# Kernel tuning notes

Hardware: AMD Instinct MI355X
Metric: run time of the kernel (lower is better)

Reference implementation:

```python
import jax, jax.numpy as jnp
import numpy as np

B, S, D, H = 4, 2048, 1024, 16
HD = D // H

def setup_inputs() -> dict:
    key = jax.random.key(0)
    ks = jax.random.split(key, 5)
    scale = 1.0 / np.sqrt(D)
    x = jax.random.normal(ks[0], (B, S, D), dtype=jnp.float32)
    w_qkv = jax.random.normal(ks[1], (D, 3 * D), dtype=jnp.float32) * scale
    b_qkv = jax.random.normal(ks[2], (3 * D,), dtype=jnp.float32) * 0.01
    w_proj = jax.random.normal(ks[3], (D, D), dtype=jnp.float32) * scale
    b_proj = jax.random.normal(ks[4], (D,), dtype=jnp.float32) * 0.01
    return {"x": x, "w_qkv": w_qkv, "b_qkv": b_qkv, "w_proj": w_proj, "b_proj": b_proj}

def reference(x, w_qkv, b_qkv, w_proj, b_proj):
    b, s, d = x.shape
    qkv = x @ w_qkv + b_qkv                      # [B,S,3D]
    qkv = qkv.reshape(b, s, 3, H, HD)
    q, k, v = jnp.moveaxis(qkv, 2, 0)            # each [B,S,H,HD]
    q = q.transpose(0, 2, 1, 3)                  # [B,H,S,HD]
    k = k.transpose(0, 2, 1, 3)
    v = v.transpose(0, 2, 1, 3)
    scale = 1.0 / jnp.sqrt(jnp.asarray(HD, dtype=x.dtype))
    scores = jnp.einsum('bhqd,bhkd->bhqk', q, k) * scale
    attn = jax.nn.softmax(scores, axis=-1)
    out = jnp.einsum('bhqk,bhkd->bhqd', attn, v)  # [B,H,S,HD]
    out = out.transpose(0, 2, 1, 3).reshape(b, s, d)
    return out @ w_proj + b_proj
```

## Files before the change

### kernel.cpp

```cpp
#include <hip/hip_runtime.h>

#define B_  4
#define S_  2048
#define D_  1024
#define H_  16
#define HD_ 64
#define M_  (B_*S_)
#define QSCALE 0.1803368801111204f

typedef unsigned short u16;
typedef __bf16 bf16x8 __attribute__((ext_vector_type(8)));
typedef __bf16 bf16x2 __attribute__((ext_vector_type(2)));
typedef float  f32x4  __attribute__((ext_vector_type(4)));
typedef float  f32x16 __attribute__((ext_vector_type(16)));

__device__ __forceinline__ u16 f2bf(float f) {
  unsigned int u = __float_as_uint(f);
  u += 0x7fffu + ((u >> 16) & 1u);
  return (u16)(u >> 16);
}
__device__ __forceinline__ unsigned int packbf2(float lo, float hi) {
#if __has_builtin(__builtin_amdgcn_cvt_pk_bf16_f32)
  union { bf16x2 v; unsigned int u; } c;
  c.v = __builtin_amdgcn_cvt_pk_bf16_f32(lo, hi);
  return c.u;
#else
  return (unsigned int)f2bf(lo) | ((unsigned int)f2bf(hi) << 16);
#endif
}
__device__ __forceinline__ void gld16(const void* g, void* l) {
  __builtin_amdgcn_global_load_lds(
      (const __attribute__((address_space(1))) unsigned int*)g,
      (__attribute__((address_space(3))) unsigned int*)l, 16, 0, 0);
}
#define WAIT_VM8() asm volatile("s_waitcnt vmcnt(8)" ::: "memory")
#define WAIT_VM0() asm volatile("s_waitcnt vmcnt(0)" ::: "memory")
#define MFMA32(a,b,c) __builtin_amdgcn_mfma_f32_32x32x16_bf16(a,b,c,0,0,0)
#define MFMA16(a,b,c) __builtin_amdgcn_mfma_f32_16x16x32_bf16(a,b,c,0,0,0)

__device__ __forceinline__ size_t off16e(int r, int k) {
  return ((size_t)((r >> 7) * 32 + (k >> 5))) * 4096
       + (size_t)((r >> 4) & 7) * 512
       + (size_t)(((k >> 3) & 3) * 16 + (r & 15)) * 8 + (k & 7);
}
__device__ __forceinline__ size_t offA32(int bh, int s, int hd) {
  return ((size_t)(bh * 32 + (s >> 6)) * 8 + ((s >> 5) & 1) * 4 + (hd >> 4)) * 512
       + (size_t)(((hd >> 3) & 1) * 32 + (s & 31)) * 8 + (hd & 7);
}
__device__ __forceinline__ size_t offVT(int bh, int s, int hd) {
  return ((size_t)(bh * 32 + (s >> 6)) * 8 + (hd >> 5) * 4 + ((s >> 4) & 3)) * 512
       + (size_t)(((s >> 3) & 1) * 32 + (hd & 31)) * 8 + (s & 7);
}

__global__ void cvt_f32_bf16(const float* __restrict__ in, u16* __restrict__ out, int n4) {
  int i = blockIdx.x * 256 + threadIdx.x;
  if (i < n4) {
    float4 v = ((const float4*)in)[i];
    int m = i >> 8;
    int k = (i & 255) * 4;
    *(uint2*)&out[off16e(m, k)] = make_uint2(packbf2(v.x, v.y), packbf2(v.z, v.w));
  }
}

__global__ void transpose_w(const float* __restrict__ in, u16* __restrict__ out, int R, int C) {
  __shared__ float tile[32][33];
  int c0 = blockIdx.x * 32, r0 = blockIdx.y * 32;
  int tx = threadIdx.x, ty = threadIdx.y;
  #pragma unroll
  for (int i = 0; i < 4; i++)
    tile[ty + i*8][tx] = in[(size_t)(r0 + ty + i*8) * C + c0 + tx];
  __syncthreads();
  #pragma unroll
  for (int i = 0; i < 4; i++)
    out[off16e(c0 + ty + i*8, r0 + tx)] = f2bf(tile[tx][ty + i*8]);
}

__global__ __launch_bounds__(256,2) void gemm_qkv(
    const u16* __restrict__ X, const u16* __restrict__ WT,
    const float* __restrict__ bias,
    u16* __restrict__ qb, u16* __restrict__ kb, u16* __restrict__ vb)
{
  __shared__ u16 As[2*8*512];
  __shared__ u16 Bs[2*8*512];
  const int t = threadIdx.x, w = t >> 6, l = t & 63;
  const int m0 = blockIdx.y * 128, n0 = blockIdx.x * 128;
  const u16* Ab = X  + (size_t)(m0 >> 7) * 32 * 4096;
  const u16* Bb = WT + (size_t)(n0 >> 7) * 32 * 4096;

  #pragma unroll
  for (int f2 = 0; f2 < 2; f2++) {
    gld16(Ab + (w*2+f2)*512 + l*8, (char*)As + (w*2+f2)*1024);
    gld16(Bb + (w*2+f2)*512 + l*8, (char*)Bs + (w*2+f2)*1024);
  }
  f32x4 acc[4][4] = {};
  const int af = (w >> 1) * 4, bf = (w & 1) * 4;
  for (int it = 0; it < 32; it++) {
    __syncthreads();
    const int cur = (it & 1) * 4096;
    if (it < 31) {
      const int nb = ((it + 1) & 1) * 8;
      const size_t gs = (size_t)(it + 1) * 4096;
      #pragma unroll
      for (int f2 = 0; f2 < 2; f2++) {
        gld16(Ab + gs + (w*2+f2)*512 + l*8, (char*)As + (nb + w*2+f2)*1024);
        gld16(Bb + gs + (w*2+f2)*512 + l*8, (char*)Bs + (nb + w*2+f2)*1024);
      }
    }
    bf16x8 a[4], b[4];
    #pragma unroll
    for (int mt = 0; mt < 4; mt++) a[mt] = *(const bf16x8*)(As + cur + (af+mt)*512 + l*8);
    #pragma unroll
    for (int nt = 0; nt < 4; nt++) b[nt] = *(const bf16x8*)(Bs + cur + (bf+nt)*512 + l*8);
    #pragma unroll
    for (int mt = 0; mt < 4; mt++)
      #pragma unroll
      for (int nt = 0; nt < 4; nt++)
        acc[mt][nt] = MFMA16(a[mt], b[nt], acc[mt][nt]);
  }
  const int wm = (w >> 1) * 64, wn = (w & 1) * 64, lr = l & 15, quad = l >> 4;
  #pragma unroll
  for (int mt = 0; mt < 4; mt++)
  #pragma unroll
  for (int nt = 0; nt < 4; nt++) {
    int n = n0 + wn + nt * 16 + lr;
    float bia = bias[n];
    int which = n >> 10, hh = (n >> 6) & 15, hd = n & 63;
    #pragma unroll
    for (int r = 0; r < 4; r++) {
      int m = m0 + wm + mt * 16 + quad * 4 + r;
      float v = acc[mt][nt][r] + bia;
      int bb = m >> 11, s = m & 2047, bh = bb * 16 + hh;
      if (which == 0)      qb[offA32(bh, s, hd)] = f2bf(v * QSCALE);
      else if (which == 1) kb[offA32(bh, s, hd)] = f2bf(v);
      else                 vb[offVT(bh, s, hd)] = f2bf(v);
    }
  }
}

__global__ __launch_bounds__(256,2) void gemm_proj(
    const u16* __restrict__ X, const u16* __restrict__ WT,
    const float* __restrict__ bias, float* __restrict__ out)
{
  __shared__ u16 As[2*8*512];
  __shared__ u16 Bs[2*8*512];
  const int t = threadIdx.x, w = t >> 6, l = t & 63;
  const int m0 = blockIdx.y * 128, n0 = blockIdx.x * 128;
  const u16* Ab = X  + (size_t)(m0 >> 7) * 32 * 4096;
  const u16* Bb = WT + (size_t)(n0 >> 7) * 32 * 4096;

  #pragma unroll
  for (int f2 = 0; f2 < 2; f2++) {
    gld16(Ab + (w*2+f2)*512 + l*8, (char*)As + (w*2+f2)*1024);
    gld16(Bb + (w*2+f2)*512 + l*8, (char*)Bs + (w*2+f2)*1024);
  }
  f32x4 acc[4][4] = {};
  const int af = (w >> 1) * 4, bf = (w & 1) * 4;
  for (int it = 0; it < 32; it++) {
    __syncthreads();
    const int cur = (it & 1) * 4096;
    if (it < 31) {
      const int nb = ((it + 1) & 1) * 8;
      const size_t gs = (size_t)(it + 1) * 4096;
      #pragma unroll
      for (int f2 = 0; f2 < 2; f2++) {
        gld16(Ab + gs + (w*2+f2)*512 + l*8, (char*)As + (nb + w*2+f2)*1024);
        gld16(Bb + gs + (w*2+f2)*512 + l*8, (char*)Bs + (nb + w*2+f2)*1024);
      }
    }
    bf16x8 a[4], b[4];
    #pragma unroll
    for (int mt = 0; mt < 4; mt++) a[mt] = *(const bf16x8*)(As + cur + (af+mt)*512 + l*8);
    #pragma unroll
    for (int nt = 0; nt < 4; nt++) b[nt] = *(const bf16x8*)(Bs + cur + (bf+nt)*512 + l*8);
    #pragma unroll
    for (int mt = 0; mt < 4; mt++)
      #pragma unroll
      for (int nt = 0; nt < 4; nt++)
        acc[mt][nt] = MFMA16(a[mt], b[nt], acc[mt][nt]);
  }
  const int wm = (w >> 1) * 64, wn = (w & 1) * 64, lr = l & 15, quad = l >> 4;
  #pragma unroll
  for (int mt = 0; mt < 4; mt++)
  #pragma unroll
  for (int nt = 0; nt < 4; nt++) {
    int n = n0 + wn + nt * 16 + lr;
    float bia = bias[n];
    #pragma unroll
    for (int r = 0; r < 4; r++) {
      int m = m0 + wm + mt * 16 + quad * 4 + r;
      out[(size_t)m * D_ + n] = acc[mt][nt][r] + bia;
    }
  }
}

__global__ __launch_bounds__(128,2) void attn(
    const u16* __restrict__ qb, const u16* __restrict__ kb,
    const u16* __restrict__ vt, u16* __restrict__ ob)
{
  __shared__ u16 Kl[2][8*512];
  __shared__ u16 Vl[2][8*512];
  __shared__ float redL[2][64];
  const int t = threadIdx.x, w = t >> 6, l = t & 63, l31 = l & 31, h = l >> 5;
  const int i = blockIdx.x, xcd = i & 7, j = i >> 3;
  const int bh = xcd * 8 + (j >> 4), qt = j & 15;
  const int b = bh >> 4, hh = bh & 15;
  const int s0 = qt * 128 + w * 64;
  const u16* qp = qb + (size_t)bh * 131072;
  const u16* kp = kb + (size_t)bh * 131072;
  const u16* vp = vt + (size_t)bh * 131072;
  u16* myK = &Kl[w][0];
  u16* myV = &Vl[w][0];

  bf16x8 qa[2][4];
  #pragma unroll
  for (int g = 0; g < 2; g++)
    #pragma unroll
    for (int kk = 0; kk < 4; kk++)
      qa[g][kk] = *(const bf16x8*)(qp + ((size_t)(qt*2 + w) * 8 + g*4 + kk) * 512 + l*8);

  f32x16 o[2][2] = {};
  float l_[2] = {0.f, 0.f};

  #pragma unroll
  for (int f = 0; f < 8; f++)
    gld16(kp + (size_t)f * 512 + l*8, (char*)myK + f*1024);

  for (int kt = 0; kt < 32; kt++) {
    const size_t gs = (size_t)kt * 4096;
    #pragma unroll
    for (int f = 0; f < 8; f++)
      gld16(vp + gs + f*512 + l*8, (char*)myV + f*1024);

    WAIT_VM8();

    f32x16 sf[2][2] = {};
    #pragma unroll
    for (int kk = 0; kk < 4; kk++) {
      bf16x8 ka0 = *(const bf16x8*)(myK + (0*4 + kk)*512 + l*8);
      bf16x8 ka1 = *(const bf16x8*)(myK + (1*4 + kk)*512 + l*8);
      sf[0][0] = MFMA32(ka0, qa[0][kk], sf[0][0]);
      sf[0][1] = MFMA32(ka0, qa[1][kk], sf[0][1]);
      sf[1][0] = MFMA32(ka1, qa[0][kk], sf[1][0]);
      sf[1][1] = MFMA32(ka1, qa[1][kk], sf[1][1]);
    }

    if (kt < 31) {
      const size_t gs2 = (size_t)(kt + 1) * 4096;
      #pragma unroll
      for (int f = 0; f < 8; f++)
        gld16(kp + gs2 + f*512 + l*8, (char*)myK + f*1024);
    }

    unsigned int pk[2][2][4][2];
    #pragma unroll
    for (int g = 0; g < 2; g++) {
      float sa = 0.f, sb = 0.f, sc = 0.f, sd = 0.f;
      #pragma unroll
      for (int mt = 0; mt < 2; mt++)
        #pragma unroll
        for (int e = 0; e < 4; e++) {
          float p0 = __builtin_amdgcn_exp2f(sf[mt][g][4*e+0]);
          float p1 = __builtin_amdgcn_exp2f(sf[mt][g][4*e+1]);
          float p2 = __builtin_amdgcn_exp2f(sf[mt][g][4*e+2]);
          float p3 = __builtin_amdgcn_exp2f(sf[mt][g][4*e+3]);
          sa += p0; sb += p1; sc += p2; sd += p3;
          pk[mt][g][e][0] = packbf2(p0, p1);
          pk[mt][g][e][1] = packbf2(p2, p3);
        }
      float s = (sa + sb) + (sc + sd);
      s += __shfl_xor(s, 32);
      l_[g] += s;
    }

    if (kt < 31) { WAIT_VM8(); }
    else         { WAIT_VM0(); }

    #pragma unroll
    for (int kk2 = 0; kk2 < 4; kk2++) {
      const int mt = kk2 >> 1, k1 = kk2 & 1;
      bf16x8 bv0 = *(const bf16x8*)(myV + (0*4 + kk2)*512 + l*8);
      bf16x8 bv1 = *(const bf16x8*)(myV + (1*4 + kk2)*512 + l*8);
      #pragma unroll
      for (int g = 0; g < 2; g++) {
        unsigned int s0_ = h ? pk[mt][g][2*k1][0] : pk[mt][g][2*k1+1][0];
        unsigned int s1_ = h ? pk[mt][g][2*k1][1] : pk[mt][g][2*k1+1][1];
        unsigned int r0 = (unsigned int)__shfl_xor((int)s0_, 32);
        unsigned int r1 = (unsigned int)__shfl_xor((int)s1_, 32);
        union { unsigned int u[4]; bf16x8 v; } pa;
        pa.u[0] = h ? r0 : pk[mt][g][2*k1][0];
        pa.u[1] = h ? r1 : pk[mt][g][2*k1][1];
        pa.u[2] = h ? pk[mt][g][2*k1+1][0] : r0;
        pa.u[3] = h ? pk[mt][g][2*k1+1][1] : r1;
        o[g][0] = MFMA32(pa.v, bv0, o[g][0]);
        o[g][1] = MFMA32(pa.v, bv1, o[g][1]);
      }
    }
  }

  #pragma unroll
  for (int g = 0; g < 2; g++) redL[w][g*32 + l31] = 1.f / l_[g];
  __syncthreads();
  #pragma unroll
  for (int g = 0; g < 2; g++)
    #pragma unroll
    for (int rb = 0; rb < 4; rb++) {
      f32x4 iv4 = *(const f32x4*)&redL[w][g*32 + 8*rb + 4*h];
      #pragma unroll
      for (int c = 0; c < 4; c++) {
        int r = rb*4 + c;
        int row = s0 + g*32 + c + 8*rb + 4*h;
        int m = b * S_ + row;
        int d0 = hh*64 + l31, d1 = hh*64 + 32 + l31;
        ob[off16e(m, d0)] = f2bf(o[g][0][r] * iv4[c]);
        ob[off16e(m, d1)] = f2bf(o[g][1][r] * iv4[c]);
      }
    }
}

extern "C" void kernel_launch(void* const* d_in, const int* in_sizes, int n_in,
                              void* d_out, int out_size, void* d_ws, size_t ws_size,
                              hipStream_t stream) {
  const float* x      = (const float*)d_in[0];
  const float* w_qkv  = (const float*)d_in[1];
  const float* b_qkv  = (const float*)d_in[2];
  const float* w_proj = (const float*)d_in[3];
  const float* b_proj = (const float*)d_in[4];
  float* out = (float*)d_out;

  char* ws = (char*)d_ws;
  u16* xbf    = (u16*)ws; ws += (size_t)M_ * D_ * 2;
  u16* wqkvT  = (u16*)ws; ws += (size_t)3 * D_ * D_ * 2;
  u16* wprojT = (u16*)ws; ws += (size_t)D_ * D_ * 2;
  u16* qbuf   = (u16*)ws; ws += (size_t)M_ * D_ * 2;
  u16* kbuf   = (u16*)ws; ws += (size_t)M_ * D_ * 2;
  u16* vtbuf  = (u16*)ws; ws += (size_t)M_ * D_ * 2;
  u16* aobuf  = (u16*)ws; ws += (size_t)M_ * D_ * 2;

  cvt_f32_bf16<<<(M_ * D_ / 4 + 255) / 256, 256, 0, stream>>>(x, xbf, M_ * D_ / 4);
  transpose_w<<<dim3(3 * D_ / 32, D_ / 32), dim3(32, 8), 0, stream>>>(w_qkv, wqkvT, D_, 3 * D_);
  transpose_w<<<dim3(D_ / 32, D_ / 32), dim3(32, 8), 0, stream>>>(w_proj, wprojT, D_, D_);
  gemm_qkv<<<dim3(3 * D_ / 128, M_ / 128), 256, 0, stream>>>(xbf, wqkvT, b_qkv, qbuf, kbuf, vtbuf);
  attn<<<1024, 128, 0, stream>>>(qbuf, kbuf, vtbuf, aobuf);
  gemm_proj<<<dim3(D_ / 128, M_ / 128), 256, 0, stream>>>(aobuf, wprojT, b_proj, out);
}
```

Measured before the change: 311.6 us.

## Share K/V tiles across four waves with double-buffered LDS in attention

```diff
diff --git a/kernel.cpp b/kernel.cpp
--- a/kernel.cpp
+++ b/kernel.cpp
@@ -193,128 +193,123 @@
   }
 }
 
-__global__ __launch_bounds__(128,2) void attn(
+__global__ __launch_bounds__(256,4) void attn(
     const u16* __restrict__ qb, const u16* __restrict__ kb,
     const u16* __restrict__ vt, u16* __restrict__ ob)
 {
-  __shared__ u16 Kl[2][8*512];
-  __shared__ u16 Vl[2][8*512];
-  __shared__ float redL[2][64];
+  __shared__ u16 Ks[2][8*512];
+  __shared__ u16 Vs[2][8*512];
+  __shared__ float redL[4][32];
   const int t = threadIdx.x, w = t >> 6, l = t & 63, l31 = l & 31, h = l >> 5;
   const int i = blockIdx.x, xcd = i & 7, j = i >> 3;
   const int bh = xcd * 8 + (j >> 4), qt = j & 15;
   const int b = bh >> 4, hh = bh & 15;
-  const int s0 = qt * 128 + w * 64;
+  const int s0 = qt * 128 + w * 32;
   const u16* qp = qb + (size_t)bh * 131072;
   const u16* kp = kb + (size_t)bh * 131072;
   const u16* vp = vt + (size_t)bh * 131072;
-  u16* myK = &Kl[w][0];
-  u16* myV = &Vl[w][0];
-
-  bf16x8 qa[2][4];
-  #pragma unroll
-  for (int g = 0; g < 2; g++)
+
+  bf16x8 qa[4];
+  {
+    const size_t qbase = ((size_t)(qt*2 + (w >> 1)) * 8 + (w & 1) * 4) * 512;
     #pragma unroll
     for (int kk = 0; kk < 4; kk++)
-      qa[g][kk] = *(const bf16x8*)(qp + ((size_t)(qt*2 + w) * 8 + g*4 + kk) * 512 + l*8);
-
-  f32x16 o[2][2] = {};
-  float l_[2] = {0.f, 0.f};
-
-  #pragma unroll
-  for (int f = 0; f < 8; f++)
-    gld16(kp + (size_t)f * 512 + l*8, (char*)myK + f*1024);
+      qa[kk] = *(const bf16x8*)(qp + qbase + (size_t)kk * 512 + l*8);
+  }
+
+  f32x16 o[2] = {};
+  float l_ = 0.f;
+
+  #pragma unroll
+  for (int c = 0; c < 2; c++) {
+    gld16(kp + (size_t)(w*2 + c) * 512 + l*8, (char*)&Ks[0][0] + (w*2 + c)*1024);
+    gld16(vp + (size_t)(w*2 + c) * 512 + l*8, (char*)&Vs[0][0] + (w*2 + c)*1024);
+  }
+  WAIT_VM0();
+  __syncthreads();
 
   for (int kt = 0; kt < 32; kt++) {
-    const size_t gs = (size_t)kt * 4096;
-    #pragma unroll
-    for (int f = 0; f < 8; f++)
-      gld16(vp + gs + f*512 + l*8, (char*)myV + f*1024);
-
-    WAIT_VM8();
-
-    f32x16 sf[2][2] = {};
+    const int cur = kt & 1, nxt = cur ^ 1;
+    const u16* Kb = &Ks[cur][0];
+    const u16* Vb = &Vs[cur][0];
+
+    if (kt < 31) {
+      const size_t gs = (size_t)(kt + 1) * 4096;
+      #pragma unroll
+      for (int c = 0; c < 2; c++) {
+        gld16(kp + gs + (size_t)(w*2 + c) * 512 + l*8, (char*)&Ks[nxt][0] + (w*2 + c)*1024);
+        gld16(vp + gs + (size_t)(w*2 + c) * 512 + l*8, (char*)&Vs[nxt][0] + (w*2 + c)*1024);
+      }
+    }
+
+    f32x16 sf[2] = {};
     #pragma unroll
     for (int kk = 0; kk < 4; kk++) {
-      bf16x8 ka0 = *(const bf16x8*)(myK + (0*4 + kk)*512 + l*8);
-      bf16x8 ka1 = *(const bf16x8*)(myK + (1*4 + kk)*512 + l*8);
-      sf[0][0] = MFMA32(ka0, qa[0][kk], sf[0][0]);
-      sf[0][1] = MFMA32(ka0, qa[1][kk], sf[0][1]);
-      sf[1][0] = MFMA32(ka1, qa[0][kk], sf[1][0]);
-      sf[1][1] = MFMA32(ka1, qa[1][kk], sf[1][1]);
-    }
-
-    if (kt < 31) {
-      const size_t gs2 = (size_t)(kt + 1) * 4096;
-      #pragma unroll
-      for (int f = 0; f < 8; f++)
-        gld16(kp + gs2 + f*512 + l*8, (char*)myK + f*1024);
-    }
-
-    unsigned int pk[2][2][4][2];
-    #pragma unroll
-    for (int g = 0; g < 2; g++) {
+      bf16x8 ka0 = *(const bf16x8*)(Kb + (0*4 + kk)*512 + l*8);
+      bf16x8 ka1 = *(const bf16x8*)(Kb + (1*4 + kk)*512 + l*8);
+      sf[0] = MFMA32(ka0, qa[kk], sf[0]);
+      sf[1] = MFMA32(ka1, qa[kk], sf[1]);
+    }
+
+    unsigned int pk[2][4][2];
+    {
       float sa = 0.f, sb = 0.f, sc = 0.f, sd = 0.f;
       #pragma unroll
       for (int mt = 0; mt < 2; mt++)
         #pragma unroll
         for (int e = 0; e < 4; e++) {
-          float p0 = __builtin_amdgcn_exp2f(sf[mt][g][4*e+0]);
-          float p1 = __builtin_amdgcn_exp2f(sf[mt][g][4*e+1]);
-          float p2 = __builtin_amdgcn_exp2f(sf[mt][g][4*e+2]);
-          float p3 = __builtin_amdgcn_exp2f(sf[mt][g][4*e+3]);
+          float p0 = __builtin_amdgcn_exp2f(sf[mt][4*e+0]);
+          float p1 = __builtin_amdgcn_exp2f(sf[mt][4*e+1]);
+          float p2 = __builtin_amdgcn_exp2f(sf[mt][4*e+2]);
+          float p3 = __builtin_amdgcn_exp2f(sf[mt][4*e+3]);
           sa += p0; sb += p1; sc += p2; sd += p3;
-          pk[mt][g][e][0] = packbf2(p0, p1);
-          pk[mt][g][e][1] = packbf2(p2, p3);
+          pk[mt][e][0] = packbf2(p0, p1);
+          pk[mt][e][1] = packbf2(p2, p3);
         }
       float s = (sa + sb) + (sc + sd);
       s += __shfl_xor(s, 32);
-      l_[g] += s;
-    }
-
-    if (kt < 31) { WAIT_VM8(); }
-    else         { WAIT_VM0(); }
+      l_ += s;
+    }
 
     #pragma unroll
     for (int kk2 = 0; kk2 < 4; kk2++) {
       const int mt = kk2 >> 1, k1 = kk2 & 1;
-      bf16x8 bv0 = *(const bf16x8*)(myV + (0*4 + kk2)*512 + l*8);
-      bf16x8 bv1 = *(const bf16x8*)(myV + (1*4 + kk2)*512 + l*8);
-      #pragma unroll
-      for (int g = 0; g < 2; g++) {
-        unsigned int s0_ = h ? pk[mt][g][2*k1][0] : pk[mt][g][2*k1+1][0];
-        unsigned int s1_ = h ? pk[mt][g][2*k1][1] : pk[mt][g][2*k1+1][1];
-        unsigned int r0 = (unsigned int)__shfl_xor((int)s0_, 32);
-        unsigned int r1 = (unsigned int)__shfl_xor((int)s1_, 32);
-        union { unsigned int u[4]; bf16x8 v; } pa;
-        pa.u[0] = h ? r0 : pk[mt][g][2*k1][0];
-        pa.u[1] = h ? r1 : pk[mt][g][2*k1][1];
-        pa.u[2] = h ? pk[mt][g][2*k1+1][0] : r0;
-        pa.u[3] = h ? pk[mt][g][2*k1+1][1] : r1;
-        o[g][0] = MFMA32(pa.v, bv0, o[g][0]);
-        o[g][1] = MFMA32(pa.v, bv1, o[g][1]);
-      }
-    }
-  }
-
-  #pragma unroll
-  for (int g = 0; g < 2; g++) redL[w][g*32 + l31] = 1.f / l_[g];
+      bf16x8 bv0 = *(const bf16x8*)(Vb + (0*4 + kk2)*512 + l*8);
+      bf16x8 bv1 = *(const bf16x8*)(Vb + (1*4 + kk2)*512 + l*8);
+      unsigned int s0_ = h ? pk[mt][2*k1][0] : pk[mt][2*k1+1][0];
+      unsigned int s1_ = h ? pk[mt][2*k1][1] : pk[mt][2*k1+1][1];
+      unsigned int r0 = (unsigned int)__shfl_xor((int)s0_, 32);
+      unsigned int r1 = (unsigned int)__shfl_xor((int)s1_, 32);
+      union { unsigned int u[4]; bf16x8 v; } pa;
+      pa.u[0] = h ? r0 : pk[mt][2*k1][0];
+      pa.u[1] = h ? r1 : pk[mt][2*k1][1];
+      pa.u[2] = h ? pk[mt][2*k1+1][0] : r0;
+      pa.u[3] = h ? pk[mt][2*k1+1][1] : r1;
+      o[0] = MFMA32(pa.v, bv0, o[0]);
+      o[1] = MFMA32(pa.v, bv1, o[1]);
+    }
+
+    if (kt < 31) {
+      WAIT_VM0();
+      __syncthreads();
+    }
+  }
+
+  redL[w][l31] = 1.f / l_;
   __syncthreads();
   #pragma unroll
-  for (int g = 0; g < 2; g++)
-    #pragma unroll
-    for (int rb = 0; rb < 4; rb++) {
-      f32x4 iv4 = *(const f32x4*)&redL[w][g*32 + 8*rb + 4*h];
-      #pragma unroll
-      for (int c = 0; c < 4; c++) {
-        int r = rb*4 + c;
-        int row = s0 + g*32 + c + 8*rb + 4*h;
-        int m = b * S_ + row;
-        int d0 = hh*64 + l31, d1 = hh*64 + 32 + l31;
-        ob[off16e(m, d0)] = f2bf(o[g][0][r] * iv4[c]);
-        ob[off16e(m, d1)] = f2bf(o[g][1][r] * iv4[c]);
-      }
-    }
+  for (int rb = 0; rb < 4; rb++) {
+    f32x4 iv4 = *(const f32x4*)&redL[w][8*rb + 4*h];
+    #pragma unroll
+    for (int c = 0; c < 4; c++) {
+      int r = rb*4 + c;
+      int row = s0 + c + 8*rb + 4*h;
+      int m = b * S_ + row;
+      int d0 = hh*64 + l31, d1 = hh*64 + 32 + l31;
+      ob[off16e(m, d0)] = f2bf(o[0][r] * iv4[c]);
+      ob[off16e(m, d1)] = f2bf(o[1][r] * iv4[c]);
+    }
+  }
 }
 
 extern "C" void kernel_launch(void* const* d_in, const int* in_sizes, int n_in,
@@ -340,6 +335,6 @@
   transpose_w<<<dim3(3 * D_ / 32, D_ / 32), dim3(32, 8), 0, stream>>>(w_qkv, wqkvT, D_, 3 * D_);
   transpose_w<<<dim3(D_ / 32, D_ / 32), dim3(32, 8), 0, stream>>>(w_proj, wprojT, D_, D_);
   gemm_qkv<<<dim3(3 * D_ / 128, M_ / 128), 256, 0, stream>>>(xbf, wqkvT, b_qkv, qbuf, kbuf, vtbuf);
-  attn<<<1024, 128, 0, stream>>>(qbuf, kbuf, vtbuf, aobuf);
+  attn<<<1024, 256, 0, stream>>>(qbuf, kbuf, vtbuf, aobuf);
   gemm_proj<<<dim3(D_ / 128, M_ / 128), 256, 0, stream>>>(aobuf, wprojT, b_proj, out);
 }
```

Measured after the change: 318.9 us. +2.3%, slower.
